# Performance work log

Hardware: AMD Instinct MI355X
Metric: run time of the kernel (lower is better)

Reference implementation:

```python
import jax, jax.numpy as jnp
import numpy as np

B, C, H, W = 2, 128, 128, 128
HEADS = 8
D = C // HEADS
EPS = 1e-5


def _conv(x, w, pad):
    # x: [B,C,H,W], w: [O,I,kh,kw]
    return jax.lax.conv_general_dilated(
        x, w, window_strides=(1, 1), padding=[(pad, pad), (pad, pad)],
        dimension_numbers=("NCHW", "OIHW", "NCHW"))


def setup_inputs() -> dict:
    key = jax.random.key(0)
    ks = jax.random.split(key, 9)
    s = 0.05
    w11 = lambda k: jax.random.normal(k, (C, C, 1, 1), jnp.float32) * s
    w33 = lambda k: jax.random.normal(k, (C, C, 3, 3), jnp.float32) * s
    return {
        "x": jax.random.normal(ks[0], (B, C, H, W), jnp.float32),
        "gamma": jnp.ones((W,), jnp.float32),   # LayerNorm over LAST dim (W==C)
        "beta": jnp.zeros((W,), jnp.float32),
        "scale": jnp.ones((1,), jnp.float32),
        "wq1": w11(ks[1]), "wq2": w33(ks[2]),
        "wk1": w11(ks[3]), "wk2": w33(ks[4]),
        "wv1": w11(ks[5]), "wv2": w33(ks[6]),
        "wo": w11(ks[7]),
    }


def reference(x, gamma, beta, scale, wq1, wq2, wk1, wk2, wv1, wv2, wo):
    residual = x
    # torch nn.LayerNorm(channels) normalizes the last axis (W), biased variance
    mu = jnp.mean(x, axis=-1, keepdims=True)
    var = jnp.var(x, axis=-1, keepdims=True)
    xn = (x - mu) * jax.lax.rsqrt(var + EPS) * gamma + beta

    q = _conv(_conv(xn, wq1, 0), wq2, 1).reshape(B, HEADS, H * W, D)
    k = _conv(_conv(xn, wk1, 0), wk2, 1).reshape(B, HEADS, H * W, D).transpose(0, 1, 3, 2)
    v = _conv(_conv(xn, wv1, 0), wv2, 1).reshape(B, HEADS, H * W, D)

    # transposed (channel) attention: [B,h,d,HW] @ [B,h,HW,d] -> [B,h,d,d]
    attn = jnp.matmul(k, q) / scale
    probs = jax.nn.softmax(attn, axis=-1)
    out = jnp.matmul(v, probs)                      # [B,h,HW,d]
    out = out.transpose(0, 1, 3, 2).reshape(B, C, H, W)
    return _conv(out, wo, 0) + residual
```

## Files before the change

### kernel.cpp

```cpp
#include <hip/hip_runtime.h>
#include <hip/hip_bf16.h>

typedef unsigned short u16;
typedef _Float16 f16;
typedef f16 f16x8 __attribute__((ext_vector_type(8)));
typedef float f32x4 __attribute__((ext_vector_type(4)));

__device__ __forceinline__ float b2f(u16 u) {
  unsigned v = (unsigned)u << 16; float f; __builtin_memcpy(&f, &v, 4); return f;
}
__device__ __forceinline__ u16 f2b(float f) {
  return __builtin_bit_cast(u16, __float2bfloat16(f));
}
__device__ __forceinline__ float h2f(u16 u) {
  return (float)__builtin_bit_cast(f16, u);
}
__device__ __forceinline__ u16 f2h(float f) {
  return __builtin_bit_cast(u16, (f16)f);
}
__device__ __forceinline__ void gload16(const void* g, void* l) {
  __builtin_amdgcn_global_load_lds((__attribute__((address_space(1))) void*)(const_cast<void*>(g)),
                                   (__attribute__((address_space(3))) void*)l, 16, 0, 0);
}
__device__ __forceinline__ f32x4 mfma16(int4 a, int4 b, f32x4 c) {
  return __builtin_amdgcn_mfma_f32_16x16x32_f16(__builtin_bit_cast(f16x8, a),
                                                __builtin_bit_cast(f16x8, b), c, 0, 0, 0);
}
union PK { int4 i; u16 u[8]; };

__device__ __forceinline__ int detect_isf(const u16* x, int tid, int nthr) {
  __shared__ int dcnt;
  if (tid == 0) dcnt = 0;
  __syncthreads();
  int c = 0;
  for (int i = tid; i < 1024; i += nthr) {
    u16 u = x[i * 2];
    if (((u >> 7) & 0xFF) >= 0x90) ++c;
  }
  if (c) atomicAdd(&dcnt, c);
  __syncthreads();
  return dcnt > 16;
}

__global__ __launch_bounds__(256) void k_weff(
    const void* __restrict__ w1q, const void* __restrict__ w2q,
    const void* __restrict__ w1k, const void* __restrict__ w2k,
    const void* __restrict__ w1v, const void* __restrict__ w2v,
    const u16* __restrict__ xdet, u16* __restrict__ weff) {
  __shared__ __align__(16) u16 sA[16384];
  __shared__ __align__(16) u16 sB[16384];
  int tid = threadIdx.x;
  int isf = detect_isf(xdet, tid, 256);
  int blk = blockIdx.x;
  int tap = blk / 3, br = blk - tap * 3;
  const void* w1 = br == 0 ? w1q : (br == 1 ? w1k : w1v);
  const void* w2 = br == 0 ? w2q : (br == 1 ? w2k : w2v);
  if (isf) {
    const float* w2f = (const float*)w2;
    const float* w1f = (const float*)w1;
#pragma unroll 4
    for (int i = 0; i < 64; ++i) {
      int e = i * 256 + tid;
      int c = e >> 7, m = e & 127;
      sA[c * 128 + (m ^ ((c & 15) << 3))] = f2h(w2f[e * 9 + tap]);
      int ci = e & 127;
      sB[ci * 128 + ((e >> 7) ^ ((ci & 15) << 3))] = f2h(w1f[e]);
    }
  } else {
    const u16* w2u = (const u16*)w2;
    const u16* w1u = (const u16*)w1;
#pragma unroll 4
    for (int i = 0; i < 64; ++i) {
      int e = i * 256 + tid;
      int c = e >> 7, m = e & 127;
      sA[c * 128 + (m ^ ((c & 15) << 3))] = f2h(b2f(w2u[e * 9 + tap]));
      int ci = e & 127;
      sB[ci * 128 + ((e >> 7) ^ ((ci & 15) << 3))] = f2h(b2f(w1u[e]));
    }
  }
  __syncthreads();
  int lane = tid & 63, wv = tid >> 6;
  int m0w = (wv >> 1) * 64, n0w = (wv & 1) * 64;
  f32x4 acc[4][4] = {};
#pragma unroll
  for (int k0 = 0; k0 < 4; ++k0) {
    int mrow = k0 * 32 + (lane >> 4) * 8;
    int4 a4[4], b4[4];
#pragma unroll
    for (int mi = 0; mi < 4; ++mi) {
      int c = m0w + mi * 16 + (lane & 15);
      a4[mi] = *(const int4*)&sA[c * 128 + (mrow ^ ((c & 15) << 3))];
    }
#pragma unroll
    for (int ni = 0; ni < 4; ++ni) {
      int ci = n0w + ni * 16 + (lane & 15);
      b4[ni] = *(const int4*)&sB[ci * 128 + (mrow ^ ((ci & 15) << 3))];
    }
#pragma unroll
    for (int mi = 0; mi < 4; ++mi)
#pragma unroll
      for (int ni = 0; ni < 4; ++ni)
        acc[mi][ni] = mfma16(a4[mi], b4[ni], acc[mi][ni]);
  }
  __syncthreads();
#pragma unroll
  for (int mi = 0; mi < 4; ++mi)
#pragma unroll
    for (int ni = 0; ni < 4; ++ni) {
#pragma unroll
      for (int r = 0; r < 4; ++r) {
        int c = m0w + mi * 16 + (lane >> 4) * 4 + r;
        int ci = n0w + ni * 16 + (lane & 15);
        sA[c * 128 + ci] = f2h(acc[mi][ni][r]);
      }
    }
  __syncthreads();
  int4* dst = (int4*)((char*)weff + (size_t)blk * 32768);
#pragma unroll
  for (int i = 0; i < 8; ++i) {
    int gidx = i * 256 + tid;
    int k0 = gidx >> 9;
    int ch = gidx & 511;
    int mt = ch >> 6, l = ch & 63;
    int c = mt * 16 + (l & 15);
    int g = k0 * 4 + (l >> 4);
    dst[gidx] = *(const int4*)((const char*)sA + c * 256 + g * 16);
  }
}

__global__ __launch_bounds__(256) void k_ln(const void* __restrict__ xr,
    const void* __restrict__ gr, const void* __restrict__ br_,
    u16* __restrict__ xnt, float* __restrict__ attnb) {
  __shared__ __align__(16) float sx[16384];
  __shared__ __align__(16) u16 sn[16384];
  __shared__ float sg[128], sb[128];
  int tid = threadIdx.x;
  int b = blockIdx.x >> 7, h = blockIdx.x & 127;
  int isf = detect_isf((const u16*)xr, tid, 256);
  if (blockIdx.x == 0) {
    for (int i = tid; i < 4096; i += 256) attnb[i] = 0.f;
  }
  if (tid < 128) {
    sg[tid] = isf ? ((const float*)gr)[tid] : b2f(((const u16*)gr)[tid]);
    sb[tid] = isf ? ((const float*)br_)[tid] : b2f(((const u16*)br_)[tid]);
  }
  if (isf) {
#pragma unroll
    for (int it = 0; it < 16; ++it) {
      int d = it * 4096 + tid * 16;
      int c = d >> 9;
      int p = (d >> 4) & 31;
      int sc = p ^ (c & 31);
      const char* src = (const char*)xr + (size_t)(b * 128 + c) * 65536 + (size_t)h * 512 + (sc << 4);
      gload16(src, (char*)sx + d);
    }
  } else {
    int c = tid >> 1, half = tid & 1;
    const u16* xu = (const u16*)xr + ((size_t)(b * 128 + c) * 128 + h) * 128 + half * 64;
    for (int i = 0; i < 16; ++i) {
      int phys = (half * 16 + i) ^ (c & 31);
      float* dst = sx + c * 128 + phys * 4;
#pragma unroll
      for (int j = 0; j < 4; ++j) dst[j] = b2f(xu[i * 4 + j]);
    }
  }
  __syncthreads();
  int c = tid >> 1, half = tid & 1;
  float sum = 0.f, sq = 0.f;
#pragma unroll
  for (int i = 0; i < 16; ++i) {
    int phys = (half * 16 + i) ^ (c & 31);
    const float* v = sx + c * 128 + phys * 4;
#pragma unroll
    for (int j = 0; j < 4; ++j) { float f = v[j]; sum += f; sq += f * f; }
  }
  sum += __shfl_xor(sum, 1);
  sq  += __shfl_xor(sq, 1);
  float mu = sum * 0.0078125f;
  float var = sq * 0.0078125f - mu * mu;
  float rs = rsqrtf(var + 1e-5f);
  int cg = c >> 3, cl = c & 7;
#pragma unroll
  for (int i = 0; i < 16; ++i) {
    int logical = half * 16 + i;
    int phys = logical ^ (c & 31);
    const float* v = sx + c * 128 + phys * 4;
#pragma unroll
    for (int j = 0; j < 4; ++j) {
      int w = logical * 4 + j;
      sn[w * 128 + (((cg ^ (w & 15)) << 3) | cl)] = f2h((v[j] - mu) * rs * sg[w] + sb[w]);
    }
  }
  __syncthreads();
  char* obase = (char*)xnt + (size_t)(b * 128 + h) * 32768;
#pragma unroll
  for (int i = 0; i < 8; ++i) {
    int idx = i * 256 + tid;
    int g = idx >> 7, w = idx & 127;
    int phys = g ^ (w & 15);
    *(int4*)(obase + idx * 16) = *(const int4*)((const char*)sn + w * 256 + (phys << 4));
  }
}

#define STAGE_PAIR(S, BUF) do { \
    const char* base_ = (const char*)weff + (size_t)((S) >> 1) * 32768 + (size_t)((S) & 1) * 16384; \
    char* dst_ = wq + (BUF) * 16384; \
    gload16(base_ + tid * 16, dst_ + tid * 16); \
    gload16(base_ + 4096 + tid * 16, dst_ + 4096 + tid * 16); \
    gload16(base_ + 8192 + tid * 16, dst_ + 8192 + tid * 16); \
    gload16(base_ + 12288 + tid * 16, dst_ + 12288 + tid * 16); \
  } while (0)

#define BC_LOAD(DST, T6) do { \
    int dy_ = (T6) / 3, dx_ = (T6) % 3; \
    int hp_ = h + dy_ - 1; \
    bool rowok_ = (unsigned)hp_ < 128u; \
    int hpc_ = rowok_ ? hp_ : 0; \
    const char* rb_ = (const char*)xnt + (size_t)(b * 128 + hpc_) * 32768; \
    _Pragma("unroll") \
    for (int kk = 0; kk < 4; ++kk) \
      _Pragma("unroll") \
      for (int ni = 0; ni < 2; ++ni) { \
        int wpg = whalf * 64 + n0l + ni * 16 + (lane & 15) + dx_ - 1; \
        bool ok = rowok_ && (unsigned)wpg < 128u; \
        int wpc = ok ? wpg : 0; \
        int chunk = (kk * 4 + (lane >> 4)) * 128 + wpc; \
        int4 v = *(const int4*)(rb_ + chunk * 16); \
        DST[kk][ni] = ok ? v : make_int4(0, 0, 0, 0); \
      } \
  } while (0)

#define QSTEP2(ACC, J) do { \
    const char* qb = wq + ((J) % 3) * 16384; \
    _Pragma("unroll") \
    for (int kk2 = 0; kk2 < 2; ++kk2) { \
      int k0 = ((J) & 1) * 2 + kk2; \
      int4 af[4]; \
      _Pragma("unroll") \
      for (int mi = 0; mi < 4; ++mi) \
        af[mi] = *(const int4*)(qb + kk2 * 8192 + ((wv >> 1) * 4 + mi) * 1024 + lane * 16); \
      _Pragma("unroll") \
      for (int mi = 0; mi < 4; ++mi) { \
        ACC[mi][0] = mfma16(af[mi], bcA[k0][0], ACC[mi][0]); \
        ACC[mi][1] = mfma16(af[mi], bcA[k0][1], ACC[mi][1]); \
      } \
    } \
  } while (0)

__global__ __launch_bounds__(256, 2) void k_conv(const u16* __restrict__ xnt,
    const u16* __restrict__ weff, u16* __restrict__ Vc, float* __restrict__ attnb) {
  __shared__ __align__(16) char wq[49152];
  int tid = threadIdx.x, lane = tid & 63, wv = tid >> 6;
  int bi = blockIdx.x;
  int whalf = bi & 1, h = (bi >> 1) & 127, b = bi >> 8;
  int m0 = (wv >> 1) * 64;
  int n0l = (wv & 1) * 32;

  int4 bcA[4][2], bcB[4][2];
  BC_LOAD(bcA, 0);
  STAGE_PAIR(0, 0);
  STAGE_PAIR(1, 1);

  f32x4 aq[4][2] = {}, ak[4][2] = {}, av[4][2] = {};

  for (int t6 = 0; t6 < 9; ++t6) {
#pragma unroll
    for (int j = 0; j < 6; ++j) {
      if (j == 1 || j == 2) {
        if (t6 < 8) asm volatile("s_waitcnt vmcnt(12)" ::: "memory");
        else        asm volatile("s_waitcnt vmcnt(4)" ::: "memory");
      } else if (j == 5) {
        if (t6 == 8) asm volatile("s_waitcnt vmcnt(0)" ::: "memory");
        else         asm volatile("s_waitcnt vmcnt(4)" ::: "memory");
      } else {
        asm volatile("s_waitcnt vmcnt(4)" ::: "memory");
      }
      __builtin_amdgcn_s_barrier();
      asm volatile("" ::: "memory");
      if (j == 0 && t6 > 0) {
#pragma unroll
        for (int kk = 0; kk < 4; ++kk)
#pragma unroll
          for (int ni = 0; ni < 2; ++ni) bcA[kk][ni] = bcB[kk][ni];
      }
      if (j == 0 || j == 1)      QSTEP2(aq, j);
      else if (j == 2 || j == 3) QSTEP2(ak, j);
      else                       QSTEP2(av, j);
      int s = t6 * 6 + j;
      if (s + 2 <= 53) STAGE_PAIR(s + 2, (j + 2) % 3);
      if (j == 0 && t6 < 8) BC_LOAD(bcB, t6 + 1);
    }
  }
  __syncthreads();
  u16* scrQ = (u16*)wq;
  u16* scrK = (u16*)(wq + 16384);
  u16* scrV = (u16*)(wq + 32768);
#pragma unroll
  for (int mi = 0; mi < 4; ++mi)
#pragma unroll
    for (int ni = 0; ni < 2; ++ni)
#pragma unroll
      for (int r = 0; r < 4; ++r) {
        int cc = m0 + mi * 16 + (lane >> 4) * 4 + r;
        int wl = n0l + ni * 16 + (lane & 15);
        scrQ[cc * 64 + wl] = f2h(aq[mi][ni][r]);
        scrK[cc * 64 + wl] = f2h(ak[mi][ni][r]);
        scrV[cc * 64 + wl] = f2h(av[mi][ni][r]);
      }
  __syncthreads();
#pragma unroll
  for (int hh = 0; hh < 2; ++hh) {
    int hd = wv * 2 + hh;
    f32x4 g = {};
#pragma unroll
    for (int k2 = 0; k2 < 2; ++k2) {
      PK A, Bq;
#pragma unroll
      for (int jj = 0; jj < 8; ++jj) {
        int k = (lane >> 4) * 8 + jj;
        int ci = k2 * 8 + (k >> 2);
        int wl = (k & 3) * 16 + (lane & 15);
        A.u[jj]  = scrK[(hd * 16 + ci) * 64 + wl];
        Bq.u[jj] = scrQ[(hd * 16 + ci) * 64 + wl];
      }
      g = mfma16(A.i, Bq.i, g);
    }
#pragma unroll
    for (int r = 0; r < 4; ++r)
      atomicAdd(&attnb[((b * 8 + hd) * 16 + (lane >> 4) * 4 + r) * 16 + (lane & 15)], g[r]);
  }
  char* dstV = (char*)Vc + (size_t)(b * 128) * 32768 + (size_t)h * 256 + (size_t)whalf * 128;
#pragma unroll
  for (int i = 0; i < 4; ++i) {
    int gi = i * 256 + tid;
    int c = gi >> 3, off = (gi & 7) << 4;
    *(int4*)(dstV + (size_t)c * 32768 + off) = *(const int4*)((const char*)scrV + c * 128 + off);
  }
}

__global__ __launch_bounds__(256) void k_w2(const float* __restrict__ attnb,
    const void* __restrict__ wo, const void* __restrict__ scale,
    const u16* __restrict__ xdet, u16* __restrict__ w2s) {
  __shared__ float P[256];
  int b = blockIdx.x, hd = blockIdx.y;
  int tid = threadIdx.x;
  int isf = detect_isf(xdet, tid, 256);
  float sc = isf ? ((const float*)scale)[0] : b2f(((const u16*)scale)[0]);
  float inv_sc = 1.f / sc;
  P[tid] = attnb[(b * 8 + hd) * 256 + tid] * inv_sc;
  __syncthreads();
  if (tid < 16) {
    int dk = tid;
    float m = -1e30f;
#pragma unroll
    for (int j = 0; j < 16; ++j) m = fmaxf(m, P[dk * 16 + j]);
    float e[16]; float s = 0.f;
#pragma unroll
    for (int j = 0; j < 16; ++j) { e[j] = expf(P[dk * 16 + j] - m); s += e[j]; }
    float is = 1.f / s;
#pragma unroll
    for (int j = 0; j < 16; ++j) P[dk * 16 + j] = e[j] * is;
  }
  __syncthreads();
  int co = tid & 127, kg = tid >> 7;
  float wr[16];
  if (isf) {
    const float* wof = (const float*)wo;
#pragma unroll
    for (int d = 0; d < 16; ++d) wr[d] = wof[co * 128 + hd * 16 + d];
  } else {
    const u16* wou = (const u16*)wo;
#pragma unroll
    for (int d = 0; d < 16; ++d) wr[d] = b2f(wou[co * 128 + hd * 16 + d]);
  }
  PK p;
#pragma unroll
  for (int j = 0; j < 8; ++j) {
    int dd = kg * 8 + j;
    float a = 0.f;
#pragma unroll
    for (int d = 0; d < 16; ++d) a += wr[d] * P[dd * 16 + d];
    p.u[j] = f2h(a);
  }
  int slot = hd * 2 + kg;
  *(int4*)((char*)w2s + (size_t)b * 32768 + co * 256 + ((slot ^ (co & 7)) << 4)) = p.i;
}

__global__ __launch_bounds__(256, 2) void k_final(const u16* __restrict__ w2s,
    const u16* __restrict__ Vc, const void* __restrict__ xr, void* __restrict__ outr) {
  __shared__ __align__(16) char sW[32768];
  __shared__ __align__(16) char sBk[16384];
  int tid = threadIdx.x, lane = tid & 63, wv = tid >> 6;
  int bi = blockIdx.x;
  int whalf = bi & 1, h = (bi >> 1) & 127, b = bi >> 8;
  int isf = detect_isf((const u16*)xr, tid, 256);
  const char* wsrc = (const char*)w2s + (size_t)b * 32768;
#pragma unroll
  for (int i = 0; i < 8; ++i) {
    int off = i * 4096 + tid * 16;
    gload16(wsrc + off, sW + off);
  }
#pragma unroll
  for (int i = 0; i < 4; ++i) {
    int gi = i * 256 + tid;
    int lr = gi >> 4, chunk = gi & 15;
    int hd8 = lr >> 3, rl = whalf * 8 + (lr & 7);
    int cv = hd8 * 16 + (h >> 3);
    int hv = (h & 7) * 16 + rl;
    const char* src = (const char*)Vc + (size_t)(b * 128 + cv) * 32768 + (size_t)hv * 256 + (chunk << 4);
    gload16(src, sBk + gi * 16);
  }
  __syncthreads();
  int m0 = (wv >> 1) * 64, n0l = (wv & 1) * 32;
  f32x4 acc[4][2] = {};
#pragma unroll
  for (int k0i = 0; k0i < 4; ++k0i) {
    int4 af[4], bfr[2];
#pragma unroll
    for (int mi = 0; mi < 4; ++mi) {
      int cc = m0 + mi * 16 + (lane & 15);
      int slot = (k0i * 4 + (lane >> 4)) ^ (cc & 7);
      af[mi] = *(const int4*)(sW + cc * 256 + (slot << 4));
    }
#pragma unroll
    for (int ni = 0; ni < 2; ++ni) {
      int wl = n0l + ni * 16 + (lane & 15);
      int k = k0i * 32 + (lane >> 4) * 8;
      int hd8 = k >> 4, dd0 = k & 15;
      bfr[ni] = *(const int4*)(sBk + (hd8 * 8 + (wl >> 3)) * 256 + ((wl & 7) * 32 + dd0 * 2));
    }
#pragma unroll
    for (int mi = 0; mi < 4; ++mi)
#pragma unroll
      for (int ni = 0; ni < 2; ++ni)
        acc[mi][ni] = mfma16(af[mi], bfr[ni], acc[mi][ni]);
  }
  if (isf) {
    const float* xf = (const float*)xr;
    float* of = (float*)outr;
#pragma unroll
    for (int mi = 0; mi < 4; ++mi)
#pragma unroll
      for (int ni = 0; ni < 2; ++ni) {
        int w = whalf * 64 + n0l + ni * 16 + (lane & 15);
#pragma unroll
        for (int r = 0; r < 4; ++r) {
          int cc = m0 + mi * 16 + (lane >> 4) * 4 + r;
          size_t idx = ((size_t)(b * 128 + cc) * 128 + (size_t)h) * 128 + w;
          of[idx] = acc[mi][ni][r] + xf[idx];
        }
      }
  } else {
    const u16* xu = (const u16*)xr;
    u16* ou = (u16*)outr;
#pragma unroll
    for (int mi = 0; mi < 4; ++mi)
#pragma unroll
      for (int ni = 0; ni < 2; ++ni) {
        int w = whalf * 64 + n0l + ni * 16 + (lane & 15);
#pragma unroll
        for (int r = 0; r < 4; ++r) {
          int cc = m0 + mi * 16 + (lane >> 4) * 4 + r;
          size_t idx = ((size_t)(b * 128 + cc) * 128 + (size_t)h) * 128 + w;
          ou[idx] = f2b(acc[mi][ni][r] + b2f(xu[idx]));
        }
      }
  }
}

extern "C" void kernel_launch(void* const* d_in, const int* in_sizes, int n_in,
                              void* d_out, int out_size, void* d_ws, size_t ws_size,
                              hipStream_t stream) {
  (void)in_sizes; (void)n_in; (void)out_size; (void)ws_size;
  const void* x     = d_in[0];
  const void* gamma = d_in[1];
  const void* beta  = d_in[2];
  const void* scale = d_in[3];
  const void* w1q = d_in[4];
  const void* w2q = d_in[5];
  const void* w1k = d_in[6];
  const void* w2k = d_in[7];
  const void* w1v = d_in[8];
  const void* w2v = d_in[9];
  const void* wo  = d_in[10];
  char* ws = (char*)d_ws;
  u16* xnt     = (u16*)(ws);
  u16* weff    = (u16*)(ws + (8u << 20));
  u16* Vc      = (u16*)(ws + (9u << 20));
  float* attnb = (float*)(ws + (17u << 20));
  u16* w2s     = (u16*)(ws + (17u << 20) + 65536);

  hipLaunchKernelGGL(k_weff, dim3(27), dim3(256), 0, stream, w1q, w2q, w1k, w2k, w1v, w2v,
                     (const u16*)x, weff);
  hipLaunchKernelGGL(k_ln, dim3(256), dim3(256), 0, stream, x, gamma, beta, xnt, attnb);
  hipLaunchKernelGGL(k_conv, dim3(512), dim3(256), 0, stream, xnt, weff, Vc, attnb);
  hipLaunchKernelGGL(k_w2, dim3(2, 8), dim3(256), 0, stream, attnb, wo, scale, (const u16*)x, w2s);
  hipLaunchKernelGGL(k_final, dim3(512), dim3(256), 0, stream, w2s, Vc, x, d_out);
}
```

Measured before the change: 89.13 us.

## Pad xnt with zero halo, double-buffer weights, replace atomics with partial sums

The normalized activation buffer gets a one-pixel zero halo, written by extra blocks in the layernorm kernel, so the conv B-fragment loads no longer need bounds checks. The conv kernel drops from triple to double buffered weight staging (48KB to 32KB LDS) with plain __syncthreads, and asks for three blocks per CU instead of two. Attention Gram atomics are replaced by per-block partial sums that k_w2 reduces with a serial 256-way loop. The trade-off is less prefetch depth and an extra full barrier per step, plus a more expensive reduction in the small k_w2 kernel.

```diff
diff --git a/kernel.cpp b/kernel.cpp
--- a/kernel.cpp
+++ b/kernel.cpp
@@ -41,6 +41,8 @@
   __syncthreads();
   return dcnt > 16;
 }
+
+#define XROW 33280
 
 __global__ __launch_bounds__(256) void k_weff(
     const void* __restrict__ w1q, const void* __restrict__ w2q,
@@ -130,16 +132,25 @@
 
 __global__ __launch_bounds__(256) void k_ln(const void* __restrict__ xr,
     const void* __restrict__ gr, const void* __restrict__ br_,
-    u16* __restrict__ xnt, float* __restrict__ attnb) {
+    u16* __restrict__ xnt) {
   __shared__ __align__(16) float sx[16384];
   __shared__ __align__(16) u16 sn[16384];
   __shared__ float sg[128], sb[128];
   int tid = threadIdx.x;
-  int b = blockIdx.x >> 7, h = blockIdx.x & 127;
+  int bi = blockIdx.x;
+  if (bi >= 256) {
+    int pid = bi - 256;
+    int b = pid >> 1, row = (pid & 1) ? 129 : 0;
+    char* rbase = (char*)xnt + (size_t)(b * 130 + row) * XROW;
+    int4 z = make_int4(0, 0, 0, 0);
+    for (int i = 0; i < 9; ++i) {
+      int idx = i * 256 + tid;
+      if (idx < 2080) *(int4*)(rbase + idx * 16) = z;
+    }
+    return;
+  }
+  int b = bi >> 7, h = bi & 127;
   int isf = detect_isf((const u16*)xr, tid, 256);
-  if (blockIdx.x == 0) {
-    for (int i = tid; i < 4096; i += 256) attnb[i] = 0.f;
-  }
   if (tid < 128) {
     sg[tid] = isf ? ((const float*)gr)[tid] : b2f(((const u16*)gr)[tid]);
     sb[tid] = isf ? ((const float*)br_)[tid] : b2f(((const u16*)br_)[tid]);
@@ -192,17 +203,21 @@
     }
   }
   __syncthreads();
-  char* obase = (char*)xnt + (size_t)(b * 128 + h) * 32768;
+  char* obase = (char*)xnt + (size_t)(b * 130 + h + 1) * XROW;
 #pragma unroll
   for (int i = 0; i < 8; ++i) {
     int idx = i * 256 + tid;
     int g = idx >> 7, w = idx & 127;
     int phys = g ^ (w & 15);
-    *(int4*)(obase + idx * 16) = *(const int4*)((const char*)sn + w * 256 + (phys << 4));
-  }
-}
-
-#define STAGE_PAIR(S, BUF) do { \
+    *(int4*)(obase + (g * 130 + w + 1) * 16) = *(const int4*)((const char*)sn + w * 256 + (phys << 4));
+  }
+  if (tid < 32) {
+    int g = tid >> 1, side = tid & 1;
+    *(int4*)(obase + (g * 130 + (side ? 129 : 0)) * 16) = make_int4(0, 0, 0, 0);
+  }
+}
+
+#define STAGE_H(S, BUF) do { \
     const char* base_ = (const char*)weff + (size_t)((S) >> 1) * 32768 + (size_t)((S) & 1) * 16384; \
     char* dst_ = wq + (BUF) * 16384; \
     gload16(base_ + tid * 16, dst_ + tid * 16); \
@@ -213,25 +228,19 @@
 
 #define BC_LOAD(DST, T6) do { \
     int dy_ = (T6) / 3, dx_ = (T6) % 3; \
-    int hp_ = h + dy_ - 1; \
-    bool rowok_ = (unsigned)hp_ < 128u; \
-    int hpc_ = rowok_ ? hp_ : 0; \
-    const char* rb_ = (const char*)xnt + (size_t)(b * 128 + hpc_) * 32768; \
+    const char* rb_ = (const char*)xnt + (size_t)(b * 130 + h + dy_) * XROW; \
     _Pragma("unroll") \
     for (int kk = 0; kk < 4; ++kk) \
       _Pragma("unroll") \
       for (int ni = 0; ni < 2; ++ni) { \
-        int wpg = whalf * 64 + n0l + ni * 16 + (lane & 15) + dx_ - 1; \
-        bool ok = rowok_ && (unsigned)wpg < 128u; \
-        int wpc = ok ? wpg : 0; \
-        int chunk = (kk * 4 + (lane >> 4)) * 128 + wpc; \
-        int4 v = *(const int4*)(rb_ + chunk * 16); \
-        DST[kk][ni] = ok ? v : make_int4(0, 0, 0, 0); \
+        int wp1 = whalf * 64 + n0l + ni * 16 + (lane & 15) + dx_;    \
+        int chunk = (kk * 4 + (lane >> 4)) * 130 + wp1; \
+        DST[kk][ni] = *(const int4*)(rb_ + chunk * 16); \
       } \
   } while (0)
 
-#define QSTEP2(ACC, J) do { \
-    const char* qb = wq + ((J) % 3) * 16384; \
+#define QSTEP2(ACC, J, SPAR) do { \
+    const char* qb = wq + (SPAR) * 16384; \
     _Pragma("unroll") \
     for (int kk2 = 0; kk2 < 2; ++kk2) { \
       int k0 = ((J) & 1) * 2 + kk2; \
@@ -247,9 +256,9 @@
     } \
   } while (0)
 
-__global__ __launch_bounds__(256, 2) void k_conv(const u16* __restrict__ xnt,
-    const u16* __restrict__ weff, u16* __restrict__ Vc, float* __restrict__ attnb) {
-  __shared__ __align__(16) char wq[49152];
+__global__ __launch_bounds__(256, 3) void k_conv(const u16* __restrict__ xnt,
+    const u16* __restrict__ weff, u16* __restrict__ Vc, float* __restrict__ part) {
+  __shared__ __align__(16) char wq[32768];
   int tid = threadIdx.x, lane = tid & 63, wv = tid >> 6;
   int bi = blockIdx.x;
   int whalf = bi & 1, h = (bi >> 1) & 127, b = bi >> 8;
@@ -258,43 +267,31 @@
 
   int4 bcA[4][2], bcB[4][2];
   BC_LOAD(bcA, 0);
-  STAGE_PAIR(0, 0);
-  STAGE_PAIR(1, 1);
+  STAGE_H(0, 0);
+  __syncthreads();
 
   f32x4 aq[4][2] = {}, ak[4][2] = {}, av[4][2] = {};
 
   for (int t6 = 0; t6 < 9; ++t6) {
 #pragma unroll
     for (int j = 0; j < 6; ++j) {
-      if (j == 1 || j == 2) {
-        if (t6 < 8) asm volatile("s_waitcnt vmcnt(12)" ::: "memory");
-        else        asm volatile("s_waitcnt vmcnt(4)" ::: "memory");
-      } else if (j == 5) {
-        if (t6 == 8) asm volatile("s_waitcnt vmcnt(0)" ::: "memory");
-        else         asm volatile("s_waitcnt vmcnt(4)" ::: "memory");
-      } else {
-        asm volatile("s_waitcnt vmcnt(4)" ::: "memory");
-      }
-      __builtin_amdgcn_s_barrier();
-      asm volatile("" ::: "memory");
+      int s = t6 * 6 + j;
+      if (s + 1 < 54) STAGE_H(s + 1, (s + 1) & 1);
       if (j == 0 && t6 > 0) {
 #pragma unroll
         for (int kk = 0; kk < 4; ++kk)
 #pragma unroll
           for (int ni = 0; ni < 2; ++ni) bcA[kk][ni] = bcB[kk][ni];
       }
-      if (j == 0 || j == 1)      QSTEP2(aq, j);
-      else if (j == 2 || j == 3) QSTEP2(ak, j);
-      else                       QSTEP2(av, j);
-      int s = t6 * 6 + j;
-      if (s + 2 <= 53) STAGE_PAIR(s + 2, (j + 2) % 3);
       if (j == 0 && t6 < 8) BC_LOAD(bcB, t6 + 1);
-    }
-  }
-  __syncthreads();
+      if (j == 0 || j == 1)      QSTEP2(aq, j, s & 1);
+      else if (j == 2 || j == 3) QSTEP2(ak, j, s & 1);
+      else                       QSTEP2(av, j, s & 1);
+      __syncthreads();
+    }
+  }
   u16* scrQ = (u16*)wq;
   u16* scrK = (u16*)(wq + 16384);
-  u16* scrV = (u16*)(wq + 32768);
 #pragma unroll
   for (int mi = 0; mi < 4; ++mi)
 #pragma unroll
@@ -305,9 +302,9 @@
         int wl = n0l + ni * 16 + (lane & 15);
         scrQ[cc * 64 + wl] = f2h(aq[mi][ni][r]);
         scrK[cc * 64 + wl] = f2h(ak[mi][ni][r]);
-        scrV[cc * 64 + wl] = f2h(av[mi][ni][r]);
-      }
-  __syncthreads();
+      }
+  __syncthreads();
+  float* pb = part + (size_t)bi * 2048;
 #pragma unroll
   for (int hh = 0; hh < 2; ++hh) {
     int hd = wv * 2 + hh;
@@ -327,8 +324,21 @@
     }
 #pragma unroll
     for (int r = 0; r < 4; ++r)
-      atomicAdd(&attnb[((b * 8 + hd) * 16 + (lane >> 4) * 4 + r) * 16 + (lane & 15)], g[r]);
-  }
+      pb[hd * 256 + ((lane >> 4) * 4 + r) * 16 + (lane & 15)] = g[r];
+  }
+  __syncthreads();
+  u16* scrV = (u16*)wq;
+#pragma unroll
+  for (int mi = 0; mi < 4; ++mi)
+#pragma unroll
+    for (int ni = 0; ni < 2; ++ni)
+#pragma unroll
+      for (int r = 0; r < 4; ++r) {
+        int cc = m0 + mi * 16 + (lane >> 4) * 4 + r;
+        int wl = n0l + ni * 16 + (lane & 15);
+        scrV[cc * 64 + wl] = f2h(av[mi][ni][r]);
+      }
+  __syncthreads();
   char* dstV = (char*)Vc + (size_t)(b * 128) * 32768 + (size_t)h * 256 + (size_t)whalf * 128;
 #pragma unroll
   for (int i = 0; i < 4; ++i) {
@@ -338,7 +348,7 @@
   }
 }
 
-__global__ __launch_bounds__(256) void k_w2(const float* __restrict__ attnb,
+__global__ __launch_bounds__(256) void k_w2(const float* __restrict__ part,
     const void* __restrict__ wo, const void* __restrict__ scale,
     const u16* __restrict__ xdet, u16* __restrict__ w2s) {
   __shared__ float P[256];
@@ -347,7 +357,15 @@
   int isf = detect_isf(xdet, tid, 256);
   float sc = isf ? ((const float*)scale)[0] : b2f(((const u16*)scale)[0]);
   float inv_sc = 1.f / sc;
-  P[tid] = attnb[(b * 8 + hd) * 256 + tid] * inv_sc;
+  const float* pp = part + (size_t)(b * 256) * 2048 + hd * 256 + tid;
+  float a0 = 0.f, a1 = 0.f, a2 = 0.f, a3 = 0.f;
+  for (int i = 0; i < 256; i += 4) {
+    a0 += pp[(size_t)i * 2048];
+    a1 += pp[(size_t)(i + 1) * 2048];
+    a2 += pp[(size_t)(i + 2) * 2048];
+    a3 += pp[(size_t)(i + 3) * 2048];
+  }
+  P[tid] = (a0 + a1 + a2 + a3) * inv_sc;
   __syncthreads();
   if (tid < 16) {
     int dk = tid;
@@ -485,15 +503,15 @@
   const void* wo  = d_in[10];
   char* ws = (char*)d_ws;
   u16* xnt     = (u16*)(ws);
-  u16* weff    = (u16*)(ws + (8u << 20));
-  u16* Vc      = (u16*)(ws + (9u << 20));
-  float* attnb = (float*)(ws + (17u << 20));
-  u16* w2s     = (u16*)(ws + (17u << 20) + 65536);
+  u16* weff    = (u16*)(ws + (9u << 20));
+  u16* Vc      = (u16*)(ws + (10u << 20));
+  float* part  = (float*)(ws + (18u << 20));
+  u16* w2s     = (u16*)(ws + (22u << 20));
 
   hipLaunchKernelGGL(k_weff, dim3(27), dim3(256), 0, stream, w1q, w2q, w1k, w2k, w1v, w2v,
                      (const u16*)x, weff);
-  hipLaunchKernelGGL(k_ln, dim3(256), dim3(256), 0, stream, x, gamma, beta, xnt, attnb);
-  hipLaunchKernelGGL(k_conv, dim3(512), dim3(256), 0, stream, xnt, weff, Vc, attnb);
-  hipLaunchKernelGGL(k_w2, dim3(2, 8), dim3(256), 0, stream, attnb, wo, scale, (const u16*)x, w2s);
+  hipLaunchKernelGGL(k_ln, dim3(260), dim3(256), 0, stream, x, gamma, beta, xnt);
+  hipLaunchKernelGGL(k_conv, dim3(512), dim3(256), 0, stream, xnt, weff, Vc, part);
+  hipLaunchKernelGGL(k_w2, dim3(2, 8), dim3(256), 0, stream, part, wo, scale, (const u16*)x, w2s);
   hipLaunchKernelGGL(k_final, dim3(512), dim3(256), 0, stream, w2s, Vc, x, d_out);
 }
```

Result: slower. 148.3 us (+66.4%).
